# Optimization experiments

Measured on AMD Instinct MI355X. Metric: run time of the kernel, lower is better.

## Reference

```python
import jax, jax.numpy as jnp
import numpy as np
import math

D_MODEL, D_FF, N_EXPERTS, TOP_K, N_SHARED = 1024, 4096, 8, 2, 1
B, T = 4, 1024
SCALE = 1.0 / math.sqrt(N_SHARED + TOP_K / N_EXPERTS)


def setup_inputs() -> dict:
    key = jax.random.key(0)
    ks = jax.random.split(key, 10)
    s1 = 1.0 / math.sqrt(D_MODEL)
    s2 = 1.0 / math.sqrt(D_FF)
    return {
        "x": jax.random.normal(ks[0], (B, T, D_MODEL), dtype=jnp.float32),
        "w_router": jax.random.normal(ks[1], (N_EXPERTS, D_MODEL), dtype=jnp.float32) * s1,
        "W1": jax.random.normal(ks[2], (N_EXPERTS, D_FF, D_MODEL), dtype=jnp.float32) * s1,
        "b1": jax.random.normal(ks[3], (N_EXPERTS, D_FF), dtype=jnp.float32) * 0.02,
        "W2": jax.random.normal(ks[4], (N_EXPERTS, D_MODEL, D_FF), dtype=jnp.float32) * s2,
        "b2": jax.random.normal(ks[5], (N_EXPERTS, D_MODEL), dtype=jnp.float32) * 0.02,
        "Ws1": jax.random.normal(ks[6], (D_FF, D_MODEL), dtype=jnp.float32) * s1,
        "bs1": jax.random.normal(ks[7], (D_FF,), dtype=jnp.float32) * 0.02,
        "Ws2": jax.random.normal(ks[8], (D_MODEL, D_FF), dtype=jnp.float32) * s2,
        "bs2": jax.random.normal(ks[9], (D_MODEL,), dtype=jnp.float32) * 0.02,
    }


def reference(x, w_router, W1, b1, W2, b2, Ws1, bs1, Ws2, bs2):
    # Router: logits -> softmax -> top-k gate values (no renormalization, matching source)
    logits = jnp.einsum("btd,ed->bte", x, w_router)      # [B,T,E]
    probs = jax.nn.softmax(logits, axis=-1)
    vals, idx = jax.lax.top_k(probs, TOP_K)               # [B,T,K]
    # Scatter top-k gate values into dense per-expert gates [B,T,E]
    gates = jnp.sum(jax.nn.one_hot(idx, N_EXPERTS, dtype=x.dtype) * vals[..., None], axis=-2)

    # Shared (always-on) expert FFN
    hs = jax.nn.gelu(jnp.einsum("btd,fd->btf", x, Ws1) + bs1)
    acc = jnp.einsum("btf,df->btd", hs, Ws2) + bs2

    # Routed experts, densified combine: sum_e gate[b,t,e] * FFN_e(x[b,t])
    h = jax.nn.gelu(jnp.einsum("btd,efd->btef", x, W1) + b1)   # [B,T,E,F]
    y = jnp.einsum("btef,edf->bted", h, W2) + b2               # [B,T,E,D]
    acc = acc + jnp.einsum("bted,bte->btd", y, gates)

    return SCALE * acc
```

## Files before the change

### kernel.cpp

```cpp
#include <hip/hip_runtime.h>
#include <hip/hip_bf16.h>

#define NTOK 4096
#define DM   1024
#define DF   4096
#define ROWS_TOTAL 12288
#define BM 128
#define BN 128
#define BK 64
#define SCALE_F 0.8944271909999159f
#define PMAX 103

typedef __attribute__((ext_vector_type(8))) short short8;
typedef __attribute__((ext_vector_type(4))) float floatx4;

#define GLD16(gp, lp) __builtin_amdgcn_global_load_lds( \
    (const __attribute__((address_space(1))) void*)(gp), \
    (__attribute__((address_space(3))) void*)(lp), 16, 0, 0)

__device__ __forceinline__ ushort f2bf(float f){
    __hip_bfloat16 h = __float2bfloat16(f);
    return *reinterpret_cast<ushort*>(&h);
}

__device__ __forceinline__ float gelu_tanh(float v){
    float u2 = -1.5957691216057308f * (v + 0.044715f * v * v * v);
    return v / (1.0f + __expf(u2));
}

#define CVT_N0 1048576u
#define CVT_N1 9437184u
#define CVT_N2 17825792u
#define CVT_N3 18874368u
#define CVT_N4 19922944u
__global__ __launch_bounds__(256) void cvt_all(
    const float* __restrict__ x,  const float* __restrict__ W1,
    const float* __restrict__ W2, const float* __restrict__ Ws1,
    const float* __restrict__ Ws2,
    ushort* __restrict__ xb,  ushort* __restrict__ w1b, ushort* __restrict__ w2b,
    ushort* __restrict__ ws1b, ushort* __restrict__ ws2b)
{
    unsigned i = blockIdx.x * 256u + threadIdx.x;
    const float* s; ushort* d; unsigned off;
    if      (i < CVT_N0){ s = x;   d = xb;   off = i; }
    else if (i < CVT_N1){ s = W1;  d = w1b;  off = i - CVT_N0; }
    else if (i < CVT_N2){ s = W2;  d = w2b;  off = i - CVT_N1; }
    else if (i < CVT_N3){ s = Ws1; d = ws1b; off = i - CVT_N2; }
    else                { s = Ws2; d = ws2b; off = i - CVT_N3; }
    float4 v = reinterpret_cast<const float4*>(s)[off];
    ushort4 o = { f2bf(v.x), f2bf(v.y), f2bf(v.z), f2bf(v.w) };
    reinterpret_cast<ushort4*>(d)[off] = o;
}

__global__ __launch_bounds__(256) void router_kernel(
    const float* __restrict__ x, const float* __restrict__ wr,
    int* __restrict__ te, float* __restrict__ tg, int* __restrict__ tokarr)
{
    const int token = blockIdx.x * 4 + (threadIdx.x >> 6);
    const int lane  = threadIdx.x & 63;
    const float* xp = x + (size_t)token * DM;
    float s[8];
    #pragma unroll
    for (int e = 0; e < 8; e++) s[e] = 0.f;
    for (int d = lane; d < DM; d += 64){
        float xv = xp[d];
        #pragma unroll
        for (int e = 0; e < 8; e++) s[e] += xv * wr[e * DM + d];
    }
    #pragma unroll
    for (int e = 0; e < 8; e++){
        float v = s[e];
        #pragma unroll
        for (int off = 32; off > 0; off >>= 1) v += __shfl_down(v, off);
        s[e] = v;
    }
    if (lane == 0){
        float m = s[0];
        #pragma unroll
        for (int e = 1; e < 8; e++) m = fmaxf(m, s[e]);
        float p[8]; float sum = 0.f;
        #pragma unroll
        for (int e = 0; e < 8; e++){ p[e] = __expf(s[e] - m); sum += p[e]; }
        float inv = 1.f / sum;
        #pragma unroll
        for (int e = 0; e < 8; e++) p[e] *= inv;
        int i1 = 0; float p1 = p[0];
        #pragma unroll
        for (int e = 1; e < 8; e++) if (p[e] > p1){ p1 = p[e]; i1 = e; }
        int i2 = -1; float p2 = -1.f;
        #pragma unroll
        for (int e = 0; e < 8; e++) if (e != i1 && p[e] > p2){ p2 = p[e]; i2 = e; }
        te[token*2+0] = i1; te[token*2+1] = i2;
        tg[token*2+0] = p1; tg[token*2+1] = p2;
        tokarr[token] = token;
    }
}

__global__ __launch_bounds__(256) void plan_kernel(
    const int* __restrict__ te, int* __restrict__ tokarr,
    int* __restrict__ rowof, int* __restrict__ meta)
{
    __shared__ int lc[9], lcur[9];
    const int t = threadIdx.x;
    if (t < 9) lc[t] = 0;
    __syncthreads();
    for (int j = t; j < NTOK*2; j += 256) atomicAdd(&lc[te[j]], 1);
    __syncthreads();
    if (t == 0){
        int off = NTOK;
        for (int e = 0; e < 8; e++){
            lcur[e]    = off;
            meta[e]    = lc[e];
            meta[16+e] = off;
            meta[32+e] = (lc[e] + BM - 1) / BM;
            off += lc[e];
        }
        meta[8]    = NTOK;
        meta[16+8] = 0;
        meta[32+8] = NTOK / BM;
    }
    __syncthreads();
    for (int j = t; j < NTOK*2; j += 256){
        int e = te[j];
        int p = atomicAdd(&lcur[e], 1);
        tokarr[p] = j >> 1;
        rowof[j]  = p;
    }
}

template<int MODE>
__global__ __launch_bounds__(256) void gemm_kernel(
    const ushort* __restrict__ Abase,
    const ushort* __restrict__ Wb, const ushort* __restrict__ Wsb,
    const float* __restrict__ brout, const float* __restrict__ bsh,
    const int* __restrict__ meta, const int* __restrict__ tokarr,
    ushort* __restrict__ Hout, float* __restrict__ Yout)
{
    const int xcd = blockIdx.x & 7;
    const int q   = blockIdx.x >> 3;
    const int NTG = (MODE == 0) ? 4 : 1;

    int e = -1, r = 0, a0 = 0;
    #pragma unroll
    for (int ee = 0; ee < 9; ee++){
        int w = NTG * meta[32 + ee];
        if (e < 0 && q < a0 + w){ e = ee; r = q - a0; }
        a0 += w;
    }
    if (e < 0) return;
    const int mt_e = meta[32 + e];
    int ntg, mti;
    if (MODE == 0){ ntg = r / mt_e; mti = r - ntg * mt_e; }
    else          { ntg = 0;        mti = r; }
    const int nt   = (MODE == 0) ? (xcd + 8 * ntg) : xcd;
    const int cnt  = meta[e];
    const int base = meta[16 + e];

    const int K = (MODE == 0) ? DM : DF;
    const int N = (MODE == 0) ? DF : DM;
    const ushort* Bp  = (e < 8) ? (Wb + (size_t)e * DF * DM) : Wsb;
    const float* bias = (e < 8) ? (brout + e * N) : bsh;

    __shared__ ushort As[BM * BK];
    __shared__ ushort Bs[BN * BK];

    const int t    = threadIdx.x;
    const int lane = t & 63;
    const int wv   = t >> 6;
    const int wm   = (wv >> 1) * 64;
    const int wn   = (wv & 1) * 64;
    const int lrow = lane & 15;
    const int quad = lane >> 4;
    const int swz8 = ((lane & 7) ^ (lane >> 3)) * 8;

    const ushort* Ap[4];
    const ushort* Bpp[4];
    ushort* Alds[4];
    ushort* Blds[4];
    #pragma unroll
    for (int i = 0; i < 4; i++){
        int rin = wv * 32 + i * 8 + (lane >> 3);
        int pos = mti * BM + rin;
        int clp = (pos < cnt) ? pos : (cnt - 1);
        if (MODE == 0) Ap[i] = Abase + (size_t)tokarr[base + clp] * DM + swz8;
        else           Ap[i] = Abase + (size_t)(base + clp) * DF + swz8;
        Bpp[i]  = Bp + (size_t)(nt * BN + rin) * K + swz8;
        Alds[i] = &As[(wv * 32 + i * 8) * BK];
        Blds[i] = &Bs[(wv * 32 + i * 8) * BK];
    }

    floatx4 acc[4][4];
    #pragma unroll
    for (int mi = 0; mi < 4; mi++)
        #pragma unroll
        for (int ni = 0; ni < 4; ni++)
            acc[mi][ni] = (floatx4){0.f, 0.f, 0.f, 0.f};

    for (int k0 = 0; k0 < K; k0 += BK){
        __syncthreads();
        #pragma unroll
        for (int i = 0; i < 4; i++){
            GLD16(Ap[i]  + k0, Alds[i]);
            GLD16(Bpp[i] + k0, Blds[i]);
        }
        __syncthreads();
        #pragma unroll
        for (int kk = 0; kk < BK; kk += 32){
            short8 af[4], bfr[4];
            #pragma unroll
            for (int mi = 0; mi < 4; mi++){
                int row  = wm + mi * 16 + lrow;
                int phys = ((kk >> 3) + quad) ^ (row & 7);
                af[mi] = *reinterpret_cast<const short8*>(&As[row * BK + phys * 8]);
            }
            #pragma unroll
            for (int ni = 0; ni < 4; ni++){
                int row  = wn + ni * 16 + lrow;
                int phys = ((kk >> 3) + quad) ^ (row & 7);
                bfr[ni] = *reinterpret_cast<const short8*>(&Bs[row * BK + phys * 8]);
            }
            #pragma unroll
            for (int mi = 0; mi < 4; mi++)
                #pragma unroll
                for (int ni = 0; ni < 4; ni++)
                    acc[mi][ni] = __builtin_amdgcn_mfma_f32_16x16x32_bf16(af[mi], bfr[ni], acc[mi][ni], 0, 0, 0);
        }
    }

    float bv[4];
    #pragma unroll
    for (int ni = 0; ni < 4; ni++) bv[ni] = bias[nt * BN + wn + ni*16 + lrow];

    #pragma unroll
    for (int mi = 0; mi < 4; mi++){
        #pragma unroll
        for (int rg = 0; rg < 4; rg++){
            int s   = wm + mi*16 + quad*4 + rg;
            int pos = mti * BM + s;
            if (pos >= cnt) continue;
            int rr = base + pos;
            if (MODE == 0){
                ushort* hp = Hout + (size_t)rr * DF + nt * BN;
                #pragma unroll
                for (int ni = 0; ni < 4; ni++){
                    float v = acc[mi][ni][rg] + bv[ni];
                    hp[wn + ni*16 + lrow] = f2bf(gelu_tanh(v));
                }
            } else {
                float* yp = Yout + (size_t)rr * DM + nt * BN;
                #pragma unroll
                for (int ni = 0; ni < 4; ni++)
                    yp[wn + ni*16 + lrow] = acc[mi][ni][rg] + bv[ni];
            }
        }
    }
}

__global__ __launch_bounds__(256) void combine_kernel(
    const float* __restrict__ Y, const int* __restrict__ rowof,
    const float* __restrict__ tg, float* __restrict__ out)
{
    const int token = blockIdx.x;
    const int d4    = threadIdx.x;
    const float4* Y4 = reinterpret_cast<const float4*>(Y);
    int r1 = rowof[token*2+0], r2 = rowof[token*2+1];
    float g1 = tg[token*2+0],  g2 = tg[token*2+1];
    float4 a = Y4[(size_t)token * 256 + d4];
    float4 b = Y4[(size_t)r1 * 256 + d4];
    float4 c = Y4[(size_t)r2 * 256 + d4];
    float4 o;
    o.x = SCALE_F * (a.x + g1*b.x + g2*c.x);
    o.y = SCALE_F * (a.y + g1*b.y + g2*c.y);
    o.z = SCALE_F * (a.z + g1*b.z + g2*c.z);
    o.w = SCALE_F * (a.w + g1*b.w + g2*c.w);
    reinterpret_cast<float4*>(out)[(size_t)token * 256 + d4] = o;
}

extern "C" void kernel_launch(void* const* d_in, const int* in_sizes, int n_in,
                              void* d_out, int out_size, void* d_ws, size_t ws_size,
                              hipStream_t stream) {
    const float* x   = (const float*)d_in[0];
    const float* wr  = (const float*)d_in[1];
    const float* W1  = (const float*)d_in[2];
    const float* b1  = (const float*)d_in[3];
    const float* W2  = (const float*)d_in[4];
    const float* b2  = (const float*)d_in[5];
    const float* Ws1 = (const float*)d_in[6];
    const float* bs1 = (const float*)d_in[7];
    const float* Ws2 = (const float*)d_in[8];
    const float* bs2 = (const float*)d_in[9];
    float* out = (float*)d_out;

    char* ws = (char*)d_ws;
    size_t off = 0;
    auto wsalloc = [&](size_t bytes) -> char* {
        char* p = ws + off;
        off += (bytes + 255) & ~(size_t)255;
        return p;
    };
    ushort* xb   = (ushort*)wsalloc((size_t)NTOK * DM * 2);
    ushort* w1b  = (ushort*)wsalloc((size_t)8 * DF * DM * 2);
    ushort* w2b  = (ushort*)wsalloc((size_t)8 * DM * DF * 2);
    ushort* ws1b = (ushort*)wsalloc((size_t)DF * DM * 2);
    ushort* ws2b = (ushort*)wsalloc((size_t)DM * DF * 2);
    ushort* H    = (ushort*)wsalloc((size_t)ROWS_TOTAL * DF * 2);
    int*    tokarr = (int*)wsalloc(ROWS_TOTAL * 4);
    int*    rowof  = (int*)wsalloc(NTOK * 2 * 4);
    int*    te     = (int*)wsalloc(NTOK * 2 * 4);
    float*  tg     = (float*)wsalloc(NTOK * 2 * 4);
    int*    meta   = (int*)wsalloc(64 * 4);
    float*  Y = (float*)w1b;

    cvt_all<<<CVT_N4/256, 256, 0, stream>>>(x, W1, W2, Ws1, Ws2,
                                            xb, w1b, w2b, ws1b, ws2b);
    router_kernel<<<NTOK/4, 256, 0, stream>>>(x, wr, te, tg, tokarr);
    plan_kernel<<<1, 256, 0, stream>>>(te, tokarr, rowof, meta);

    gemm_kernel<0><<<8 * 4 * PMAX, 256, 0, stream>>>(xb, w1b, ws1b, b1, bs1,
        meta, tokarr, H, Y);
    gemm_kernel<1><<<8 * PMAX, 256, 0, stream>>>(H, w2b, ws2b, b2, bs2,
        meta, tokarr, H, Y);

    combine_kernel<<<NTOK, 256, 0, stream>>>(Y, rowof, tg, out);
}
```

Before: 724.8 us.

## Double-buffer LDS tiles in grouped GEMM and widen fp32-to-bf16 conversion

New measurement: 817.0 us. 12.7% more time.

```diff
diff --git a/kernel.cpp b/kernel.cpp
--- a/kernel.cpp
+++ b/kernel.cpp
@@ -28,11 +28,11 @@
     return v / (1.0f + __expf(u2));
 }
 
-#define CVT_N0 1048576u
-#define CVT_N1 9437184u
-#define CVT_N2 17825792u
-#define CVT_N3 18874368u
-#define CVT_N4 19922944u
+#define CV8_N0 524288u
+#define CV8_N1 4718592u
+#define CV8_N2 8912896u
+#define CV8_N3 9437184u
+#define CV8_N4 9961472u
 __global__ __launch_bounds__(256) void cvt_all(
     const float* __restrict__ x,  const float* __restrict__ W1,
     const float* __restrict__ W2, const float* __restrict__ Ws1,
@@ -42,14 +42,20 @@
 {
     unsigned i = blockIdx.x * 256u + threadIdx.x;
     const float* s; ushort* d; unsigned off;
-    if      (i < CVT_N0){ s = x;   d = xb;   off = i; }
-    else if (i < CVT_N1){ s = W1;  d = w1b;  off = i - CVT_N0; }
-    else if (i < CVT_N2){ s = W2;  d = w2b;  off = i - CVT_N1; }
-    else if (i < CVT_N3){ s = Ws1; d = ws1b; off = i - CVT_N2; }
-    else                { s = Ws2; d = ws2b; off = i - CVT_N3; }
-    float4 v = reinterpret_cast<const float4*>(s)[off];
-    ushort4 o = { f2bf(v.x), f2bf(v.y), f2bf(v.z), f2bf(v.w) };
-    reinterpret_cast<ushort4*>(d)[off] = o;
+    if      (i < CV8_N0){ s = x;   d = xb;   off = i; }
+    else if (i < CV8_N1){ s = W1;  d = w1b;  off = i - CV8_N0; }
+    else if (i < CV8_N2){ s = W2;  d = w2b;  off = i - CV8_N1; }
+    else if (i < CV8_N3){ s = Ws1; d = ws1b; off = i - CV8_N2; }
+    else                { s = Ws2; d = ws2b; off = i - CV8_N3; }
+    const float4* s4 = reinterpret_cast<const float4*>(s) + 2 * (size_t)off;
+    float4 a = s4[0];
+    float4 b = s4[1];
+    short8 o;
+    o[0] = (short)f2bf(a.x); o[1] = (short)f2bf(a.y);
+    o[2] = (short)f2bf(a.z); o[3] = (short)f2bf(a.w);
+    o[4] = (short)f2bf(b.x); o[5] = (short)f2bf(b.y);
+    o[6] = (short)f2bf(b.z); o[7] = (short)f2bf(b.w);
+    reinterpret_cast<short8*>(d)[off] = o;
 }
 
 __global__ __launch_bounds__(256) void router_kernel(
@@ -161,8 +167,8 @@
     const ushort* Bp  = (e < 8) ? (Wb + (size_t)e * DF * DM) : Wsb;
     const float* bias = (e < 8) ? (brout + e * N) : bsh;
 
-    __shared__ ushort As[BM * BK];
-    __shared__ ushort Bs[BN * BK];
+    __shared__ ushort As[2][BM * BK];
+    __shared__ ushort Bs[2][BN * BK];
 
     const int t    = threadIdx.x;
     const int lane = t & 63;
@@ -175,8 +181,8 @@
 
     const ushort* Ap[4];
     const ushort* Bpp[4];
-    ushort* Alds[4];
-    ushort* Blds[4];
+    ushort* Alds0[4]; ushort* Alds1[4];
+    ushort* Blds0[4]; ushort* Blds1[4];
     #pragma unroll
     for (int i = 0; i < 4; i++){
         int rin = wv * 32 + i * 8 + (lane >> 3);
@@ -184,9 +190,11 @@
         int clp = (pos < cnt) ? pos : (cnt - 1);
         if (MODE == 0) Ap[i] = Abase + (size_t)tokarr[base + clp] * DM + swz8;
         else           Ap[i] = Abase + (size_t)(base + clp) * DF + swz8;
-        Bpp[i]  = Bp + (size_t)(nt * BN + rin) * K + swz8;
-        Alds[i] = &As[(wv * 32 + i * 8) * BK];
-        Blds[i] = &Bs[(wv * 32 + i * 8) * BK];
+        Bpp[i]   = Bp + (size_t)(nt * BN + rin) * K + swz8;
+        Alds0[i] = &As[0][(wv * 32 + i * 8) * BK];
+        Alds1[i] = &As[1][(wv * 32 + i * 8) * BK];
+        Blds0[i] = &Bs[0][(wv * 32 + i * 8) * BK];
+        Blds1[i] = &Bs[1][(wv * 32 + i * 8) * BK];
     }
 
     floatx4 acc[4][4];
@@ -196,14 +204,7 @@
         for (int ni = 0; ni < 4; ni++)
             acc[mi][ni] = (floatx4){0.f, 0.f, 0.f, 0.f};
 
-    for (int k0 = 0; k0 < K; k0 += BK){
-        __syncthreads();
-        #pragma unroll
-        for (int i = 0; i < 4; i++){
-            GLD16(Ap[i]  + k0, Alds[i]);
-            GLD16(Bpp[i] + k0, Blds[i]);
-        }
-        __syncthreads();
+    auto compute = [&](const ushort* Asb, const ushort* Bsb){
         #pragma unroll
         for (int kk = 0; kk < BK; kk += 32){
             short8 af[4], bfr[4];
@@ -211,13 +212,13 @@
             for (int mi = 0; mi < 4; mi++){
                 int row  = wm + mi * 16 + lrow;
                 int phys = ((kk >> 3) + quad) ^ (row & 7);
-                af[mi] = *reinterpret_cast<const short8*>(&As[row * BK + phys * 8]);
+                af[mi] = *reinterpret_cast<const short8*>(&Asb[row * BK + phys * 8]);
             }
             #pragma unroll
             for (int ni = 0; ni < 4; ni++){
                 int row  = wn + ni * 16 + lrow;
                 int phys = ((kk >> 3) + quad) ^ (row & 7);
-                bfr[ni] = *reinterpret_cast<const short8*>(&Bs[row * BK + phys * 8]);
+                bfr[ni] = *reinterpret_cast<const short8*>(&Bsb[row * BK + phys * 8]);
             }
             #pragma unroll
             for (int mi = 0; mi < 4; mi++)
@@ -225,6 +226,37 @@
                 for (int ni = 0; ni < 4; ni++)
                     acc[mi][ni] = __builtin_amdgcn_mfma_f32_16x16x32_bf16(af[mi], bfr[ni], acc[mi][ni], 0, 0, 0);
         }
+    };
+
+    #pragma unroll
+    for (int i = 0; i < 4; i++){
+        GLD16(Ap[i], Alds0[i]);
+        GLD16(Bpp[i], Blds0[i]);
+    }
+    asm volatile("s_waitcnt vmcnt(0)" ::: "memory");
+    __builtin_amdgcn_s_barrier();
+
+    #pragma unroll 1
+    for (int k0 = 0; k0 < K; k0 += 2 * BK){
+        #pragma unroll
+        for (int i = 0; i < 4; i++){
+            GLD16(Ap[i]  + k0 + BK, Alds1[i]);
+            GLD16(Bpp[i] + k0 + BK, Blds1[i]);
+        }
+        compute(As[0], Bs[0]);
+        asm volatile("s_waitcnt vmcnt(0)" ::: "memory");
+        __builtin_amdgcn_s_barrier();
+
+        if (k0 + 2 * BK < K){
+            #pragma unroll
+            for (int i = 0; i < 4; i++){
+                GLD16(Ap[i]  + k0 + 2 * BK, Alds0[i]);
+                GLD16(Bpp[i] + k0 + 2 * BK, Blds0[i]);
+            }
+        }
+        compute(As[1], Bs[1]);
+        asm volatile("s_waitcnt vmcnt(0)" ::: "memory");
+        __builtin_amdgcn_s_barrier();
     }
 
     float bv[4];
@@ -311,7 +343,7 @@
     int*    meta   = (int*)wsalloc(64 * 4);
     float*  Y = (float*)w1b;
 
-    cvt_all<<<CVT_N4/256, 256, 0, stream>>>(x, W1, W2, Ws1, Ws2,
+    cvt_all<<<CV8_N4/256, 256, 0, stream>>>(x, W1, W2, Ws1, Ws2,
                                             xb, w1b, w2b, ws1b, ws2b);
     router_kernel<<<NTOK/4, 256, 0, stream>>>(x, wr, te, tg, tokarr);
     plan_kernel<<<1, 256, 0, stream>>>(te, tokarr, rowof, meta);
```
